# Optimization experiments

Measured on AMD Instinct MI355X. Metric: run time of the kernel, lower is better.

The kernel has to match this reference:

```python
import jax, jax.numpy as jnp
import numpy as np
from jax import lax

B_, L_, D_ = 4, 512, 512          # batch, seq_len, in_dim (d_model)
HID, H2 = 512, 256                # hidden_dim, per-direction LSTM width
NL, DST, DCV, DIN, DTR = 3, 16, 4, 1024, 32  # layers, d_state, d_conv, d_inner, dt_rank


def _silu(x):
    return x * jax.nn.sigmoid(x)


def _layernorm(x, g, b):
    m = x.mean(-1, keepdims=True)
    v = x.var(-1, keepdims=True)
    return (x - m) / jnp.sqrt(v + 1e-5) * g + b


def _mamba(x, wi, cw, cb, xpw, dw, db, Alog, Dp, wo):
    # x: (B,L,D)
    Bsz, Ls, _ = x.shape
    xz = jnp.einsum('bld,ed->ble', x, wi)          # (B,L,2*DIN)
    xin, z = jnp.split(xz, 2, axis=-1)
    # causal depthwise conv1d (kernel DCV, left-padded)
    xpad = jnp.pad(xin, ((0, 0), (DCV - 1, 0), (0, 0)))
    u = cb + sum(xpad[:, k:k + Ls, :] * cw[:, k] for k in range(DCV))
    u = _silu(u)                                   # (B,L,DIN)
    xdbl = jnp.einsum('blc,ec->ble', u, xpw)       # (B,L,DTR+2*DST)
    dt_in = xdbl[..., :DTR]
    Bc = xdbl[..., DTR:DTR + DST]
    Cc = xdbl[..., DTR + DST:]
    dt = jax.nn.softplus(jnp.einsum('blr,cr->blc', dt_in, dw) + db)  # (B,L,DIN)
    A = -jnp.exp(Alog)                             # (DIN,DST), negative

    def step(h, inp):
        dt_t, B_t, C_t, u_t = inp                  # (B,DIN),(B,DST),(B,DST),(B,DIN)
        dA = jnp.exp(dt_t[..., None] * A)          # (B,DIN,DST)
        h = dA * h + (dt_t * u_t)[..., None] * B_t[:, None, :]
        y = jnp.einsum('bcn,bn->bc', h, C_t)
        return h, y

    h0 = jnp.zeros((Bsz, DIN, DST), x.dtype)
    _, ys = lax.scan(step, h0, (dt.transpose(1, 0, 2), Bc.transpose(1, 0, 2),
                                Cc.transpose(1, 0, 2), u.transpose(1, 0, 2)))
    y = ys.transpose(1, 0, 2) + u * Dp
    y = y * _silu(z)
    return jnp.einsum('blc,dc->bld', y, wo)


def _lstm_dir(x, wih, whh, bih, bhh, reverse):
    Bsz = x.shape[0]

    def step(carry, xt):
        h, c = carry
        g = xt @ wih.T + h @ whh.T + bih + bhh     # (B,4*H2), PyTorch gate order i,f,g,o
        i, f, gg, o = jnp.split(g, 4, axis=-1)
        c = jax.nn.sigmoid(f) * c + jax.nn.sigmoid(i) * jnp.tanh(gg)
        h = jax.nn.sigmoid(o) * jnp.tanh(c)
        return (h, c), h

    init = (jnp.zeros((Bsz, H2), x.dtype), jnp.zeros((Bsz, H2), x.dtype))
    _, hs = lax.scan(step, init, x.transpose(1, 0, 2), reverse=reverse)
    return hs.transpose(1, 0, 2)


def setup_inputs():
    key = jax.random.key(0)
    ks = jax.random.split(key, 16)
    rn = lambda k, s, sc=0.02: jax.random.normal(k, s, jnp.float32) * sc
    inp = {}
    inp['x'] = jax.random.normal(ks[0], (B_, L_, D_), jnp.float32)
    inp['in_proj_w'] = rn(ks[1], (NL, 2 * DIN, D_))
    inp['conv_w'] = rn(ks[2], (NL, DIN, DCV), 0.2)
    inp['conv_b'] = jnp.zeros((NL, DIN), jnp.float32)
    inp['x_proj_w'] = rn(ks[3], (NL, DTR + 2 * DST, DIN))
    inp['dt_proj_w'] = rn(ks[4], (NL, DIN, DTR), 0.1)
    inp['dt_proj_b'] = jnp.full((NL, DIN), -4.0, jnp.float32)
    inp['A_log'] = jnp.log(jnp.broadcast_to(jnp.arange(1, DST + 1, dtype=jnp.float32), (NL, DIN, DST)))
    inp['D_param'] = jnp.ones((NL, DIN), jnp.float32)
    inp['out_proj_w'] = rn(ks[5], (NL, D_, DIN))
    inp['ln_g'] = jnp.ones((NL, D_), jnp.float32)
    inp['ln_b'] = jnp.zeros((NL, D_), jnp.float32)
    inp['lstm_w_ih'] = rn(ks[6], (2, 4 * H2, D_), 0.05)
    inp['lstm_w_hh'] = rn(ks[7], (2, 4 * H2, H2), 0.05)
    inp['lstm_b_ih'] = jnp.zeros((2, 4 * H2), jnp.float32)
    inp['lstm_b_hh'] = jnp.zeros((2, 4 * H2), jnp.float32)
    inp['fusion_w'] = rn(ks[8], (HID, D_ + HID), 0.02)
    inp['fusion_b'] = jnp.zeros((HID,), jnp.float32)
    return inp


def reference(x, in_proj_w, conv_w, conv_b, x_proj_w, dt_proj_w, dt_proj_b, A_log,
              D_param, out_proj_w, ln_g, ln_b, lstm_w_ih, lstm_w_hh, lstm_b_ih,
              lstm_b_hh, fusion_w, fusion_b):
    m = x
    for i in range(NL):
        mo = _mamba(m, in_proj_w[i], conv_w[i], conv_b[i], x_proj_w[i],
                    dt_proj_w[i], dt_proj_b[i], A_log[i], D_param[i], out_proj_w[i])
        m = _layernorm(m + mo, ln_g[i], ln_b[i])
    lf = _lstm_dir(x, lstm_w_ih[0], lstm_w_hh[0], lstm_b_ih[0], lstm_b_hh[0], False)
    lb = _lstm_dir(x, lstm_w_ih[1], lstm_w_hh[1], lstm_b_ih[1], lstm_b_hh[1], True)
    comb = jnp.concatenate([m, lf, lb], axis=-1)   # (B,L,D_+HID)
    return comb @ fusion_w.T + fusion_b
```

## Files before the change

### kernel.cpp

```cpp
#include <hip/hip_runtime.h>
#include <math.h>

#define B_  4
#define L_  512
#define D_  512
#define DIN 1024
#define DST 16
#define DCV 4
#define DTR 32
#define NL  3
#define H2  256

typedef _Float16 __f16;
typedef __f16 f16x2 __attribute__((ext_vector_type(2)));
typedef __f16 half8 __attribute__((ext_vector_type(8)));
typedef float f32x4v __attribute__((ext_vector_type(4)));
typedef unsigned uint4v __attribute__((ext_vector_type(4)));

__device__ __forceinline__ float fast_sigmoid(float x) { return 1.f / (1.f + __expf(-x)); }
__device__ __forceinline__ float fast_tanh(float x) { return 2.f / (1.f + __expf(-2.f * x)) - 1.f; }

__device__ __forceinline__ float dot2f(unsigned a, unsigned b, float c) {
  return __builtin_amdgcn_fdot2(__builtin_bit_cast(f16x2, a),
                                __builtin_bit_cast(f16x2, b), c, false);
}
__device__ __forceinline__ unsigned packf16(float a, float b) {
  f16x2 p; p.x = (__f16)a; p.y = (__f16)b;
  return __builtin_bit_cast(unsigned, p);
}

template<bool ACC>
__global__ __launch_bounds__(256) void gemm_mfma(
    const float* __restrict__ A, const float* __restrict__ W, float* __restrict__ C,
    int M, int N, int K, int lda, int ldb, int ldc,
    const float* __restrict__ bias, const float* __restrict__ bias2)
{
  __shared__ uint4v As[1024];
  __shared__ uint4v Bs[1024];
  const int tid  = threadIdx.x;
  const int lane = tid & 63, wid = tid >> 6;
  const int wr = wid >> 1, wc = wid & 1;
  const int fr = lane & 15, fq = lane >> 4;
  const int m0 = blockIdx.y * 128, n0 = blockIdx.x * 128;
  const int srow = tid >> 3, skb = tid & 7;

  f32x4v acc[4][4] = {};
  for (int k0 = 0; k0 < K; k0 += 64) {
    const float* Abase = A + (size_t)m0 * lda + k0;
    const float* Bbase = W + (size_t)n0 * ldb + k0;
    #pragma unroll
    for (int i = 0; i < 4; ++i) {
      int row = srow + i * 32;
      const float4* pa = (const float4*)(Abase + (size_t)row * lda + skb * 8);
      const float4* pb = (const float4*)(Bbase + (size_t)row * ldb + skb * 8);
      float4 a0 = pa[0], a1 = pa[1];
      float4 b0 = pb[0], b1 = pb[1];
      uint4v ap, bp;
      ap.x = packf16(a0.x, a0.y); ap.y = packf16(a0.z, a0.w);
      ap.z = packf16(a1.x, a1.y); ap.w = packf16(a1.z, a1.w);
      bp.x = packf16(b0.x, b0.y); bp.y = packf16(b0.z, b0.w);
      bp.z = packf16(b1.x, b1.y); bp.w = packf16(b1.z, b1.w);
      As[row * 8 + (skb ^ (row & 7))] = ap;
      Bs[row * 8 + (skb ^ (row & 7))] = bp;
    }
    __syncthreads();
    #pragma unroll
    for (int ks = 0; ks < 2; ++ks) {
      half8 af[4], bf[4];
      #pragma unroll
      for (int mt = 0; mt < 4; ++mt) {
        int row = wr * 64 + mt * 16 + fr;
        int kb = ks * 4 + fq;
        af[mt] = __builtin_bit_cast(half8, As[row * 8 + (kb ^ (row & 7))]);
      }
      #pragma unroll
      for (int nt = 0; nt < 4; ++nt) {
        int row = wc * 64 + nt * 16 + fr;
        int kb = ks * 4 + fq;
        bf[nt] = __builtin_bit_cast(half8, Bs[row * 8 + (kb ^ (row & 7))]);
      }
      #pragma unroll
      for (int mt = 0; mt < 4; ++mt)
        #pragma unroll
        for (int nt = 0; nt < 4; ++nt)
          acc[mt][nt] = __builtin_amdgcn_mfma_f32_16x16x32_f16(af[mt], bf[nt], acc[mt][nt], 0, 0, 0);
    }
    __syncthreads();
  }
  #pragma unroll
  for (int nt = 0; nt < 4; ++nt) {
    int n = n0 + wc * 64 + nt * 16 + fr;
    float bv = (bias ? bias[n] : 0.f) + (bias2 ? bias2[n] : 0.f);
    #pragma unroll
    for (int mt = 0; mt < 4; ++mt) {
      #pragma unroll
      for (int r = 0; r < 4; ++r) {
        int m = m0 + wr * 64 + mt * 16 + fq * 4 + r;
        float v = acc[mt][nt][r] + bv;
        if (ACC) C[(size_t)m * ldc + n] += v; else C[(size_t)m * ldc + n] = v;
      }
    }
  }
}

template<int ACT>
__global__ __launch_bounds__(256) void gemm_nt(
    const float* __restrict__ A, const float* __restrict__ Bm, float* __restrict__ C,
    int M, int N, int K, int lda, int ldb, int ldc,
    const float* __restrict__ bias)
{
  __shared__ __align__(16) float As[16][64];
  __shared__ __align__(16) float Bs[16][64];
  const int tid = threadIdx.x;
  const int tx = tid & 15, ty = tid >> 4;
  const int m0 = blockIdx.y * 64, n0 = blockIdx.x * 64;
  const int r = tid >> 2, kq = (tid & 3) * 4;
  float acc[4][4] = {};
  for (int k0 = 0; k0 < K; k0 += 16) {
    float4 av = *(const float4*)(A  + (size_t)(m0 + r) * lda + (k0 + kq));
    float4 bv = *(const float4*)(Bm + (size_t)(n0 + r) * ldb + (k0 + kq));
    As[kq+0][r] = av.x; As[kq+1][r] = av.y; As[kq+2][r] = av.z; As[kq+3][r] = av.w;
    Bs[kq+0][r] = bv.x; Bs[kq+1][r] = bv.y; Bs[kq+2][r] = bv.z; Bs[kq+3][r] = bv.w;
    __syncthreads();
    #pragma unroll
    for (int kk = 0; kk < 16; ++kk) {
      float4 a = *(const float4*)(&As[kk][ty*4]);
      float4 b = *(const float4*)(&Bs[kk][tx*4]);
      float aa[4] = {a.x, a.y, a.z, a.w};
      float bb[4] = {b.x, b.y, b.z, b.w};
      #pragma unroll
      for (int i = 0; i < 4; ++i)
        #pragma unroll
        for (int j = 0; j < 4; ++j)
          acc[i][j] = fmaf(aa[i], bb[j], acc[i][j]);
    }
    __syncthreads();
  }
  #pragma unroll
  for (int i = 0; i < 4; ++i) {
    int m = m0 + ty*4 + i;
    float* cp = C + (size_t)m * ldc + n0 + tx*4;
    #pragma unroll
    for (int j = 0; j < 4; ++j) {
      int n = n0 + tx*4 + j;
      float v = acc[i][j];
      if (bias)  v += bias[n];
      if (ACT == 1) v = (v > 20.f) ? v : log1pf(__expf(v));
      cp[j] = v;
    }
  }
}

__global__ __launch_bounds__(256) void pad_xpw(
    const float* __restrict__ src, float* __restrict__ dst)
{
  int t = blockIdx.x * 256 + threadIdx.x;
  int r = t >> 10;
  dst[t] = (r < 64) ? src[t] : 0.f;
}

__global__ __launch_bounds__(256) void pack_whh(
    const float* __restrict__ whh, uint4* __restrict__ wpk)
{
  int idx = blockIdx.x * 256 + threadIdx.x;
  int t = idx & 511;
  int q = (idx >> 9) & 15;
  int G = (idx >> 13) & 3;
  int dir = idx >> 15;
  int j = t >> 1, ks = t & 1;
  const float* src = whh + (size_t)dir * 262144 + (size_t)(G * 256 + j) * 256 + ks * 128 + q * 8;
  float4 fa = ((const float4*)src)[0];
  float4 fb = ((const float4*)src)[1];
  uint4 pk;
  pk.x = packf16(fa.x, fa.y); pk.y = packf16(fa.z, fa.w);
  pk.z = packf16(fb.x, fb.y); pk.w = packf16(fb.z, fb.w);
  wpk[idx] = pk;
}

__global__ __launch_bounds__(256) void conv_silu(
    const float* __restrict__ xz, const float* __restrict__ cw, const float* __restrict__ cb,
    float* __restrict__ u)
{
  int t = blockIdx.x * 256 + threadIdx.x;
  int c  = t & (DIN - 1);
  int bl = t >> 10;
  int l  = bl & (L_ - 1);
  float acc = cb[c];
  #pragma unroll
  for (int k = 0; k < DCV; ++k) {
    int ls = l + k - (DCV - 1);
    if (ls >= 0)
      acc = fmaf(xz[(size_t)(bl + k - (DCV - 1)) * 2048 + c], cw[c * DCV + k], acc);
  }
  u[t] = acc * fast_sigmoid(acc);
}

__global__ __launch_bounds__(256) void scan_kernel(
    const float* __restrict__ dt, const float* __restrict__ u,
    const float* __restrict__ xdbl, const float* __restrict__ xz,
    const float* __restrict__ A_log, const float* __restrict__ Dp,
    float* __restrict__ y)
{
  int t = blockIdx.x * 256 + threadIdx.x;
  int n  = t & 15;
  int bc = t >> 4;
  int c  = bc & (DIN - 1);
  int b  = bc >> 10;
  float Ac = -__expf(A_log[c * DST + n]);
  float Dc = Dp[c];
  float h = 0.f;
  const size_t row = (size_t)b * L_;

#define DECLP(i) float dtv##i, uv##i, Bn##i, Cn##i, zv##i;
  DECLP(0) DECLP(1) DECLP(2) DECLP(3)
#define LOADP(i, l) { \
    const size_t nb_ = row + (l); \
    dtv##i = dt[nb_ * DIN + c]; \
    uv##i  = u [nb_ * DIN + c]; \
    Bn##i  = xdbl[nb_ * 128 + 32 + n]; \
    Cn##i  = xdbl[nb_ * 128 + 48 + n]; \
    zv##i  = xz[nb_ * 2048 + 1024 + c]; }
#define STEPP(i, l) { \
    float dA_ = __expf(dtv##i * Ac); \
    h = fmaf(dA_, h, (dtv##i * uv##i) * Bn##i); \
    float p_ = h * Cn##i; \
    p_ += __shfl_xor(p_, 1, 64); \
    p_ += __shfl_xor(p_, 2, 64); \
    p_ += __shfl_xor(p_, 4, 64); \
    p_ += __shfl_xor(p_, 8, 64); \
    if (n == 0) { \
      float yv_ = p_ + uv##i * Dc; \
      yv_ *= zv##i * fast_sigmoid(zv##i); \
      y[(row + (l)) * DIN + c] = yv_; \
    } }

  LOADP(0, 0) LOADP(1, 1) LOADP(2, 2) LOADP(3, 3)
  for (int l = 0; l < L_ - 4; l += 4) {
    STEPP(0, l)     LOADP(0, l + 4)
    STEPP(1, l + 1) LOADP(1, l + 5)
    STEPP(2, l + 2) LOADP(2, l + 6)
    STEPP(3, l + 3) LOADP(3, l + 7)
  }
  STEPP(0, L_ - 4) STEPP(1, L_ - 3) STEPP(2, L_ - 2) STEPP(3, L_ - 1)
#undef DECLP
#undef LOADP
#undef STEPP
}

__global__ __launch_bounds__(64) void resid_ln(
    const float* __restrict__ a, const float* __restrict__ mo,
    const float* __restrict__ g, const float* __restrict__ bta,
    float* __restrict__ outm, int ldo)
{
  int row = blockIdx.x;
  int lane = threadIdx.x;
  const float* pa = a  + (size_t)row * 512;
  const float* pb = mo + (size_t)row * 512;
  float v[8];
  float s = 0.f, s2 = 0.f;
  #pragma unroll
  for (int i = 0; i < 8; ++i) {
    float x = pa[lane + i * 64] + pb[lane + i * 64];
    v[i] = x; s += x; s2 += x * x;
  }
  #pragma unroll
  for (int off = 1; off < 64; off <<= 1) {
    s  += __shfl_xor(s,  off, 64);
    s2 += __shfl_xor(s2, off, 64);
  }
  float mean = s * (1.f / 512.f);
  float var  = s2 * (1.f / 512.f) - mean * mean;
  float rstd = rsqrtf(var + 1e-5f);
  #pragma unroll
  for (int i = 0; i < 8; ++i) {
    int cidx = lane + i * 64;
    outm[(size_t)row * ldo + cidx] = (v[i] - mean) * rstd * g[cidx] + bta[cidx];
  }
}


#define WDECL(q) uint4 W0_##q, W1_##q, W2_##q;
#define LDG1(W, G, q) W = wp[((G) * 16 + (q)) * 512 + t];
#define WLOAD(q) LDG1(W0_##q, 0, q) LDG1(W1_##q, 1, q) LDG1(W2_##q, 2, q)
#define WSTEP(q) { \
    uint4 hv = h4s[buf][(q) * 2 + ks]; \
    uint4 wv = wo_lds[(q) * 512 + t]; \
    a0 = dot2f(W0_##q.x, hv.x, a0); a0 = dot2f(W0_##q.y, hv.y, a0); \
    a0 = dot2f(W0_##q.z, hv.z, a0); a0 = dot2f(W0_##q.w, hv.w, a0); \
    a1 = dot2f(W1_##q.x, hv.x, a1); a1 = dot2f(W1_##q.y, hv.y, a1); \
    a1 = dot2f(W1_##q.z, hv.z, a1); a1 = dot2f(W1_##q.w, hv.w, a1); \
    a2 = dot2f(W2_##q.x, hv.x, a2); a2 = dot2f(W2_##q.y, hv.y, a2); \
    a2 = dot2f(W2_##q.z, hv.z, a2); a2 = dot2f(W2_##q.w, hv.w, a2); \
    a3 = dot2f(wv.x, hv.x, a3); a3 = dot2f(wv.y, hv.y, a3); \
    a3 = dot2f(wv.z, hv.z, a3); a3 = dot2f(wv.w, hv.w, a3); }
#define REP16(M) M(0) M(1) M(2) M(3) M(4) M(5) M(6) M(7) \
                 M(8) M(9) M(10) M(11) M(12) M(13) M(14) M(15)

__global__ __launch_bounds__(512, 1) void lstm_rec(
    const float* __restrict__ gx, const uint4* __restrict__ wpk,
    float* __restrict__ comb)
{
  __shared__ uint4 wo_lds[16 * 512];
  __shared__ __align__(16) uint4 h4s[2][32];
  const int dir = blockIdx.x >> 2, b = blockIdx.x & 3;
  const int t = threadIdx.x;
  const int j = t >> 1, ks = t & 1;
  const uint4* wp = wpk + (size_t)dir * 4 * 16 * 512;

  REP16(WDECL)
  REP16(WLOAD)

  #pragma unroll
  for (int q = 0; q < 16; ++q)
    wo_lds[q * 512 + t] = wp[(3 * 16 + q) * 512 + t];

  if (t < 256) ((unsigned*)h4s)[t] = 0u;
  float c_reg = 0.f;
  float* outp = comb + 512 + dir * 256;
  const float* gxb = gx + (size_t)(b * L_) * 2048 + dir * 1024;
  const int offA = (ks ? 1 : 0) * 256 + j;
  const int offB = (ks ? 3 : 2) * 256 + j;
  const int p_   = t >> 2;
  const int hidx = ((p_ >> 2) & 15) * 8 + (p_ >> 6) * 4 + (p_ & 3);
  __syncthreads();

  int buf = 0;
  const int l0 = dir ? (L_ - 1) : 0;
  float pgA = gxb[(size_t)l0 * 2048 + offA];
  float pgB = gxb[(size_t)l0 * 2048 + offB];

  for (int s = 0; s < L_; ++s) {
    const int l = dir ? (L_ - 1 - s) : s;
    float pgA_n = 0.f, pgB_n = 0.f;
    if (s + 1 < L_) {
      const int ln = dir ? (L_ - 2 - s) : (s + 1);
      pgA_n = gxb[(size_t)ln * 2048 + offA];
      pgB_n = gxb[(size_t)ln * 2048 + offB];
    }
    float a0 = 0.f, a1 = 0.f, a2 = 0.f, a3 = 0.f;
    REP16(WSTEP)
    if (ks == 0) { a0 += pgA; a2 += pgB; } else { a1 += pgA; a3 += pgB; }
    a0 += __shfl_xor(a0, 1, 64);
    a1 += __shfl_xor(a1, 1, 64);
    a2 += __shfl_xor(a2, 1, 64);
    a3 += __shfl_xor(a3, 1, 64);
    const float si = fast_sigmoid(a0);
    const float sf = fast_sigmoid(a1);
    const float tg = fast_tanh(a2);
    const float so = fast_sigmoid(a3);
    c_reg = fmaf(sf, c_reg, si * tg);
    const float hv = so * fast_tanh(c_reg);
    if (ks == 0) outp[(size_t)(b * L_ + l) * 1024 + j] = hv;
    const float hv2 = __shfl_xor(hv, 2, 64);
    if ((t & 3) == 0)
      ((unsigned*)h4s[buf ^ 1])[hidx] = packf16(hv, hv2);
    pgA = pgA_n; pgB = pgB_n;
    buf ^= 1;
    __syncthreads();
  }
}

extern "C" void kernel_launch(void* const* d_in, const int* in_sizes, int n_in,
                              void* d_out, int out_size, void* d_ws, size_t ws_size,
                              hipStream_t stream)
{
  const float* x    = (const float*)d_in[0];
  const float* wi   = (const float*)d_in[1];
  const float* cw   = (const float*)d_in[2];
  const float* cb   = (const float*)d_in[3];
  const float* xpw  = (const float*)d_in[4];
  const float* dw   = (const float*)d_in[5];
  const float* db   = (const float*)d_in[6];
  const float* Alog = (const float*)d_in[7];
  const float* Dp   = (const float*)d_in[8];
  const float* wo   = (const float*)d_in[9];
  const float* lng  = (const float*)d_in[10];
  const float* lnb  = (const float*)d_in[11];
  const float* wih  = (const float*)d_in[12];
  const float* whh  = (const float*)d_in[13];
  const float* bih  = (const float*)d_in[14];
  const float* bhh  = (const float*)d_in[15];
  const float* fw   = (const float*)d_in[16];
  const float* fb   = (const float*)d_in[17];
  float* out = (float*)d_out;

  float* F    = (float*)d_ws;
  float* xz   = F;
  float* gx   = F;
  float* u    = F + 4194304;
  float* xdbl = F + 6291456;
  float* dt   = F + 6553600;
  float* ybuf = F + 8650752;
  float* mo   = F + 10747904;
  float* mbuf = F + 11796480;
  float* comb = F + 12845056;
  uint4* wpk  = (uint4*)(F + 14942208);
  float* xpw_pad = mo;

  const int M = B_ * L_;
  dim3 blk(256);

  gemm_mfma<false><<<dim3(2048/128, M/128), blk, 0, stream>>>(
      x, wih, gx, M, 2048, 512, 512, 512, 2048, bih, bhh);
  pack_whh<<<dim3(256), blk, 0, stream>>>(whh, wpk);
  lstm_rec<<<dim3(8), dim3(512), 0, stream>>>(gx, wpk, comb);

  for (int i = 0; i < NL; ++i) {
    const float* min = (i == 0) ? x : mbuf;
    pad_xpw<<<dim3(512), blk, 0, stream>>>(xpw + (size_t)i*64*1024, xpw_pad);
    gemm_mfma<false><<<dim3(2048/128, M/128), blk, 0, stream>>>(
        min, wi + (size_t)i*2048*512, xz, M, 2048, 512, 512, 512, 2048, nullptr, nullptr);
    conv_silu<<<dim3((M*DIN)/256), blk, 0, stream>>>(
        xz, cw + (size_t)i*DIN*DCV, cb + i*DIN, u);
    gemm_mfma<false><<<dim3(1, M/128), blk, 0, stream>>>(
        u, xpw_pad, xdbl, M, 128, 1024, 1024, 1024, 128, nullptr, nullptr);
    gemm_nt<1><<<dim3(1024/64, M/64), blk, 0, stream>>>(
        xdbl, dw + (size_t)i*1024*32, dt, M, 1024, 32, 128, 32, 1024, db + i*1024);
    scan_kernel<<<dim3((B_*DIN*DST)/256), blk, 0, stream>>>(
        dt, u, xdbl, xz, Alog + (size_t)i*DIN*DST, Dp + i*DIN, ybuf);
    gemm_mfma<false><<<dim3(512/128, M/128), blk, 0, stream>>>(
        ybuf, wo + (size_t)i*512*1024, mo, M, 512, 1024, 1024, 1024, 512, nullptr, nullptr);
    if (i < NL - 1)
      resid_ln<<<dim3(M), dim3(64), 0, stream>>>(
          min, mo, lng + i*512, lnb + i*512, mbuf, 512);
    else
      resid_ln<<<dim3(M), dim3(64), 0, stream>>>(
          min, mo, lng + i*512, lnb + i*512, comb, 1024);
  }

  gemm_mfma<false><<<dim3(512/128, M/128), blk, 0, stream>>>(
      comb, fw, out, M, 512, 1024, 1024, 1024, 512, fb, nullptr);
}
```

Before: 1.575 ms.

## Split LSTM recurrence across blocks with global hidden-state exchange and grid barriers

The LSTM recurrent kernel is restructured so that each of 16 blocks owns 32 hidden units for all four batch rows of one direction, rather than each of 8 blocks handling one batch row with the full weight matrix. Each block keeps its weight slice in registers, and a 16-lane shuffle reduction replaces the pairwise split. Per-step hidden states are exchanged through global memory with atomic loads and stores, and an atomic counter acts as a per-step barrier across the 8 blocks of a direction. This spreads the serial recurrence over more compute units and removes the LDS weight reads, but it adds a global synchronisation every step. It also relies on all 16 blocks being co-resident.

```diff
diff --git a/kernel.cpp b/kernel.cpp
--- a/kernel.cpp
+++ b/kernel.cpp
@@ -163,12 +163,15 @@
     const float* __restrict__ whh, uint4* __restrict__ wpk)
 {
   int idx = blockIdx.x * 256 + threadIdx.x;
-  int t = idx & 511;
-  int q = (idx >> 9) & 15;
-  int G = (idx >> 13) & 3;
-  int dir = idx >> 15;
-  int j = t >> 1, ks = t & 1;
-  const float* src = whh + (size_t)dir * 262144 + (size_t)(G * 256 + j) * 256 + ks * 128 + q * 8;
+  int u4sel = idx & 1;
+  int lane  = (idx >> 1) & 63;
+  int w     = (idx >> 7) & 7;
+  int g     = (idx >> 10) & 3;
+  int ug    = (idx >> 12) & 7;
+  int dir   = idx >> 15;
+  int j  = ug * 32 + w * 4 + (lane >> 4);
+  int ks = lane & 15;
+  const float* src = whh + (size_t)dir * 262144 + (size_t)(g * 256 + j) * 256 + ks * 16 + u4sel * 8;
   float4 fa = ((const float4*)src)[0];
   float4 fb = ((const float4*)src)[1];
   uint4 pk;
@@ -279,84 +282,112 @@
 }
 
 
-#define WDECL(q) uint4 W0_##q, W1_##q, W2_##q;
-#define LDG1(W, G, q) W = wp[((G) * 16 + (q)) * 512 + t];
-#define WLOAD(q) LDG1(W0_##q, 0, q) LDG1(W1_##q, 1, q) LDG1(W2_##q, 2, q)
-#define WSTEP(q) { \
-    uint4 hv = h4s[buf][(q) * 2 + ks]; \
-    uint4 wv = wo_lds[(q) * 512 + t]; \
-    a0 = dot2f(W0_##q.x, hv.x, a0); a0 = dot2f(W0_##q.y, hv.y, a0); \
-    a0 = dot2f(W0_##q.z, hv.z, a0); a0 = dot2f(W0_##q.w, hv.w, a0); \
-    a1 = dot2f(W1_##q.x, hv.x, a1); a1 = dot2f(W1_##q.y, hv.y, a1); \
-    a1 = dot2f(W1_##q.z, hv.z, a1); a1 = dot2f(W1_##q.w, hv.w, a1); \
-    a2 = dot2f(W2_##q.x, hv.x, a2); a2 = dot2f(W2_##q.y, hv.y, a2); \
-    a2 = dot2f(W2_##q.z, hv.z, a2); a2 = dot2f(W2_##q.w, hv.w, a2); \
-    a3 = dot2f(wv.x, hv.x, a3); a3 = dot2f(wv.y, hv.y, a3); \
-    a3 = dot2f(wv.z, hv.z, a3); a3 = dot2f(wv.w, hv.w, a3); }
-#define REP16(M) M(0) M(1) M(2) M(3) M(4) M(5) M(6) M(7) \
-                 M(8) M(9) M(10) M(11) M(12) M(13) M(14) M(15)
+#define HDECL(b) unsigned h##b##0,h##b##1,h##b##2,h##b##3,h##b##4,h##b##5,h##b##6,h##b##7;
+#define HLOAD(b) { const unsigned* hp_ = hrow + (b)*128; \
+  h##b##0 = __hip_atomic_load(hp_+0, __ATOMIC_RELAXED, __HIP_MEMORY_SCOPE_AGENT); \
+  h##b##1 = __hip_atomic_load(hp_+1, __ATOMIC_RELAXED, __HIP_MEMORY_SCOPE_AGENT); \
+  h##b##2 = __hip_atomic_load(hp_+2, __ATOMIC_RELAXED, __HIP_MEMORY_SCOPE_AGENT); \
+  h##b##3 = __hip_atomic_load(hp_+3, __ATOMIC_RELAXED, __HIP_MEMORY_SCOPE_AGENT); \
+  h##b##4 = __hip_atomic_load(hp_+4, __ATOMIC_RELAXED, __HIP_MEMORY_SCOPE_AGENT); \
+  h##b##5 = __hip_atomic_load(hp_+5, __ATOMIC_RELAXED, __HIP_MEMORY_SCOPE_AGENT); \
+  h##b##6 = __hip_atomic_load(hp_+6, __ATOMIC_RELAXED, __HIP_MEMORY_SCOPE_AGENT); \
+  h##b##7 = __hip_atomic_load(hp_+7, __ATOMIC_RELAXED, __HIP_MEMORY_SCOPE_AGENT); }
+#define DOTG(g, Wa, Wb, b) \
+  a##g##b = dot2f(Wa.x, h##b##0, a##g##b); a##g##b = dot2f(Wa.y, h##b##1, a##g##b); \
+  a##g##b = dot2f(Wa.z, h##b##2, a##g##b); a##g##b = dot2f(Wa.w, h##b##3, a##g##b); \
+  a##g##b = dot2f(Wb.x, h##b##4, a##g##b); a##g##b = dot2f(Wb.y, h##b##5, a##g##b); \
+  a##g##b = dot2f(Wb.z, h##b##6, a##g##b); a##g##b = dot2f(Wb.w, h##b##7, a##g##b);
+#define DOTB(b) DOTG(0,W0a,W0b,b) DOTG(1,W1a,W1b,b) DOTG(2,W2a,W2b,b) DOTG(3,W3a,W3b,b)
+#define RED(a) a += __shfl_xor(a,1,64); a += __shfl_xor(a,2,64); \
+               a += __shfl_xor(a,4,64); a += __shfl_xor(a,8,64);
+#define PTW(b) { \
+    float si_ = fast_sigmoid(a0##b); \
+    float sf_ = fast_sigmoid(a1##b); \
+    float tg_ = fast_tanh(a2##b); \
+    float so_ = fast_sigmoid(a3##b); \
+    c##b = fmaf(sf_, c##b, si_ * tg_); \
+    hv##b = so_ * fast_tanh(c##b); }
 
 __global__ __launch_bounds__(512, 1) void lstm_rec(
     const float* __restrict__ gx, const uint4* __restrict__ wpk,
-    float* __restrict__ comb)
-{
-  __shared__ uint4 wo_lds[16 * 512];
-  __shared__ __align__(16) uint4 h4s[2][32];
-  const int dir = blockIdx.x >> 2, b = blockIdx.x & 3;
+    float* __restrict__ comb, unsigned* __restrict__ hst, unsigned* __restrict__ cnt)
+{
+  const int bid = blockIdx.x;
+  const int dir = bid >> 3, ug = bid & 7;
   const int t = threadIdx.x;
-  const int j = t >> 1, ks = t & 1;
-  const uint4* wp = wpk + (size_t)dir * 4 * 16 * 512;
-
-  REP16(WDECL)
-  REP16(WLOAD)
-
-  #pragma unroll
-  for (int q = 0; q < 16; ++q)
-    wo_lds[q * 512 + t] = wp[(3 * 16 + q) * 512 + t];
-
-  if (t < 256) ((unsigned*)h4s)[t] = 0u;
-  float c_reg = 0.f;
-  float* outp = comb + 512 + dir * 256;
-  const float* gxb = gx + (size_t)(b * L_) * 2048 + dir * 1024;
-  const int offA = (ks ? 1 : 0) * 256 + j;
-  const int offB = (ks ? 3 : 2) * 256 + j;
-  const int p_   = t >> 2;
-  const int hidx = ((p_ >> 2) & 15) * 8 + (p_ >> 6) * 4 + (p_ & 3);
-  __syncthreads();
-
-  int buf = 0;
-  const int l0 = dir ? (L_ - 1) : 0;
-  float pgA = gxb[(size_t)l0 * 2048 + offA];
-  float pgB = gxb[(size_t)l0 * 2048 + offB];
+  const int jl = t >> 4, ks = t & 15;
+  const int j  = ug * 32 + jl;
+
+  const uint4* wsl = wpk + ((size_t)(dir * 8 + ug) * 4096);
+  const int wi_ = (t >> 6) * 128 + (t & 63) * 2;
+  uint4 W0a = wsl[0*1024 + wi_], W0b = wsl[0*1024 + wi_ + 1];
+  uint4 W1a = wsl[1*1024 + wi_], W1b = wsl[1*1024 + wi_ + 1];
+  uint4 W2a = wsl[2*1024 + wi_], W2b = wsl[2*1024 + wi_ + 1];
+  uint4 W3a = wsl[3*1024 + wi_], W3b = wsl[3*1024 + wi_ + 1];
+
+  const int g0 = ks & 3, b0 = ks >> 2;
+  float c0 = 0.f, c1 = 0.f, c2 = 0.f, c3 = 0.f;
+  const float* gxb = gx + dir * 1024 + g0 * 256 + j;
+  float* combp = comb + 512 + dir * 256 + j;
+  unsigned* hdir = hst + (size_t)dir * 512 * 512;
+  unsigned* cdir = cnt + dir * 512;
+
+  int l = dir ? (L_ - 1) : 0;
+  const int lstep = dir ? -1 : 1;
+  float gxv = gxb[(size_t)(b0 * 512 + l) * 2048];
 
   for (int s = 0; s < L_; ++s) {
-    const int l = dir ? (L_ - 1 - s) : s;
-    float pgA_n = 0.f, pgB_n = 0.f;
+    float gxn = 0.f;
+    if (s + 1 < L_) gxn = gxb[(size_t)(b0 * 512 + l + lstep) * 2048];
+
+    float a00=0,a01=0,a02=0,a03=0, a10=0,a11=0,a12=0,a13=0,
+          a20=0,a21=0,a22=0,a23=0, a30=0,a31=0,a32=0,a33=0;
+    if (s > 0) {
+      const unsigned* hrow = hdir + (size_t)(s - 1) * 512 + ks * 8;
+      HDECL(0) HDECL(1) HDECL(2) HDECL(3)
+      HLOAD(0) HLOAD(1) HLOAD(2) HLOAD(3)
+      DOTB(0) DOTB(1) DOTB(2) DOTB(3)
+    }
+    a00 += (ks== 0)?gxv:0.f; a10 += (ks== 1)?gxv:0.f; a20 += (ks== 2)?gxv:0.f; a30 += (ks== 3)?gxv:0.f;
+    a01 += (ks== 4)?gxv:0.f; a11 += (ks== 5)?gxv:0.f; a21 += (ks== 6)?gxv:0.f; a31 += (ks== 7)?gxv:0.f;
+    a02 += (ks== 8)?gxv:0.f; a12 += (ks== 9)?gxv:0.f; a22 += (ks==10)?gxv:0.f; a32 += (ks==11)?gxv:0.f;
+    a03 += (ks==12)?gxv:0.f; a13 += (ks==13)?gxv:0.f; a23 += (ks==14)?gxv:0.f; a33 += (ks==15)?gxv:0.f;
+    RED(a00) RED(a01) RED(a02) RED(a03)
+    RED(a10) RED(a11) RED(a12) RED(a13)
+    RED(a20) RED(a21) RED(a22) RED(a23)
+    RED(a30) RED(a31) RED(a32) RED(a33)
+
+    float hv0, hv1, hv2, hv3;
+    PTW(0) PTW(1) PTW(2) PTW(3)
+
+    if (ks == 0) {
+      combp[(size_t)(0 * 512 + l) * 1024] = hv0;
+      combp[(size_t)(1 * 512 + l) * 1024] = hv1;
+      combp[(size_t)(2 * 512 + l) * 1024] = hv2;
+      combp[(size_t)(3 * 512 + l) * 1024] = hv3;
+    }
+    float hp0 = __shfl_xor(hv0, 16, 64);
+    float hp1 = __shfl_xor(hv1, 16, 64);
+    float hp2 = __shfl_xor(hv2, 16, 64);
+    float hp3 = __shfl_xor(hv3, 16, 64);
+    if (ks == 0 && !(jl & 1)) {
+      unsigned* hw = hdir + (size_t)s * 512 + (j >> 1);
+      __hip_atomic_store(hw + 0*128, packf16(hv0, hp0), __ATOMIC_RELAXED, __HIP_MEMORY_SCOPE_AGENT);
+      __hip_atomic_store(hw + 1*128, packf16(hv1, hp1), __ATOMIC_RELAXED, __HIP_MEMORY_SCOPE_AGENT);
+      __hip_atomic_store(hw + 2*128, packf16(hv2, hp2), __ATOMIC_RELAXED, __HIP_MEMORY_SCOPE_AGENT);
+      __hip_atomic_store(hw + 3*128, packf16(hv3, hp3), __ATOMIC_RELAXED, __HIP_MEMORY_SCOPE_AGENT);
+    }
     if (s + 1 < L_) {
-      const int ln = dir ? (L_ - 2 - s) : (s + 1);
-      pgA_n = gxb[(size_t)ln * 2048 + offA];
-      pgB_n = gxb[(size_t)ln * 2048 + offB];
-    }
-    float a0 = 0.f, a1 = 0.f, a2 = 0.f, a3 = 0.f;
-    REP16(WSTEP)
-    if (ks == 0) { a0 += pgA; a2 += pgB; } else { a1 += pgA; a3 += pgB; }
-    a0 += __shfl_xor(a0, 1, 64);
-    a1 += __shfl_xor(a1, 1, 64);
-    a2 += __shfl_xor(a2, 1, 64);
-    a3 += __shfl_xor(a3, 1, 64);
-    const float si = fast_sigmoid(a0);
-    const float sf = fast_sigmoid(a1);
-    const float tg = fast_tanh(a2);
-    const float so = fast_sigmoid(a3);
-    c_reg = fmaf(sf, c_reg, si * tg);
-    const float hv = so * fast_tanh(c_reg);
-    if (ks == 0) outp[(size_t)(b * L_ + l) * 1024 + j] = hv;
-    const float hv2 = __shfl_xor(hv, 2, 64);
-    if ((t & 3) == 0)
-      ((unsigned*)h4s[buf ^ 1])[hidx] = packf16(hv, hv2);
-    pgA = pgA_n; pgB = pgB_n;
-    buf ^= 1;
-    __syncthreads();
+      __threadfence();
+      __syncthreads();
+      if (t == 0) {
+        atomicAdd(&cdir[s], 1u);
+        while (__hip_atomic_load(&cdir[s], __ATOMIC_ACQUIRE, __HIP_MEMORY_SCOPE_AGENT) < 8u) {}
+      }
+      __syncthreads();
+    }
+    gxv = gxn;
+    l += lstep;
   }
 }
 
@@ -395,6 +426,8 @@
   float* mbuf = F + 11796480;
   float* comb = F + 12845056;
   uint4* wpk  = (uint4*)(F + 14942208);
+  unsigned* hst = (unsigned*)dt;
+  unsigned* cnt = (unsigned*)ybuf;
   float* xpw_pad = mo;
 
   const int M = B_ * L_;
@@ -403,7 +436,8 @@
   gemm_mfma<false><<<dim3(2048/128, M/128), blk, 0, stream>>>(
       x, wih, gx, M, 2048, 512, 512, 512, 2048, bih, bhh);
   pack_whh<<<dim3(256), blk, 0, stream>>>(whh, wpk);
-  lstm_rec<<<dim3(8), dim3(512), 0, stream>>>(gx, wpk, comb);
+  hipMemsetAsync(cnt, 0, 1024 * sizeof(unsigned), stream);
+  lstm_rec<<<dim3(16), dim3(512), 0, stream>>>(gx, wpk, comb, hst, cnt);
 
   for (int i = 0; i < NL; ++i) {
     const float* min = (i == 0) ? x : mbuf;
```

Result: slower. 5.994 ms (+280.6%).

## Feed MFMA GEMMs with fp16 operands produced by upstream kernels

Applied to the files above, without the earlier changes.

Replaces the fp32-input GEMM, which converted to fp16 while staging, with a version that reads fp16 operands directly. Producers (conv_silu, scan, resid_ln, lstm_rec) now write fp16 copies of their activations, and the weights are packed to fp16 by separate kernels each call. This halves the global traffic of GEMM operand loads and removes conversion work from the GEMM inner loop. In exchange it adds extra pack launches and weight conversion traffic on every call, and rearranges the workspace layout.

```diff
diff --git a/kernel.cpp b/kernel.cpp
--- a/kernel.cpp
+++ b/kernel.cpp
@@ -30,8 +30,8 @@
 }
 
 template<bool ACC>
-__global__ __launch_bounds__(256) void gemm_mfma(
-    const float* __restrict__ A, const float* __restrict__ W, float* __restrict__ C,
+__global__ __launch_bounds__(256) void gemm_mfma_h(
+    const __f16* __restrict__ A, const __f16* __restrict__ W, float* __restrict__ C,
     int M, int N, int K, int lda, int ldb, int ldc,
     const float* __restrict__ bias, const float* __restrict__ bias2)
 {
@@ -46,20 +46,13 @@
 
   f32x4v acc[4][4] = {};
   for (int k0 = 0; k0 < K; k0 += 64) {
-    const float* Abase = A + (size_t)m0 * lda + k0;
-    const float* Bbase = W + (size_t)n0 * ldb + k0;
+    const __f16* Ab = A + (size_t)m0 * lda + k0;
+    const __f16* Bb = W + (size_t)n0 * ldb + k0;
     #pragma unroll
     for (int i = 0; i < 4; ++i) {
       int row = srow + i * 32;
-      const float4* pa = (const float4*)(Abase + (size_t)row * lda + skb * 8);
-      const float4* pb = (const float4*)(Bbase + (size_t)row * ldb + skb * 8);
-      float4 a0 = pa[0], a1 = pa[1];
-      float4 b0 = pb[0], b1 = pb[1];
-      uint4v ap, bp;
-      ap.x = packf16(a0.x, a0.y); ap.y = packf16(a0.z, a0.w);
-      ap.z = packf16(a1.x, a1.y); ap.w = packf16(a1.z, a1.w);
-      bp.x = packf16(b0.x, b0.y); bp.y = packf16(b0.z, b0.w);
-      bp.z = packf16(b1.x, b1.y); bp.w = packf16(b1.z, b1.w);
+      uint4v ap = *(const uint4v*)(Ab + (size_t)row * lda + skb * 8);
+      uint4v bp = *(const uint4v*)(Bb + (size_t)row * ldb + skb * 8);
       As[row * 8 + (skb ^ (row & 7))] = ap;
       Bs[row * 8 + (skb ^ (row & 7))] = bp;
     }
@@ -151,12 +144,21 @@
   }
 }
 
-__global__ __launch_bounds__(256) void pad_xpw(
-    const float* __restrict__ src, float* __restrict__ dst)
+__global__ __launch_bounds__(256) void packh(
+    const float* __restrict__ src, __f16* __restrict__ dst, int n)
 {
   int t = blockIdx.x * 256 + threadIdx.x;
-  int r = t >> 10;
-  dst[t] = (r < 64) ? src[t] : 0.f;
+  if (t < n) dst[t] = (__f16)src[t];
+}
+
+__global__ __launch_bounds__(256) void pack_xpw_h(
+    const float* __restrict__ xpw, __f16* __restrict__ dst)
+{
+  int t = blockIdx.x * 256 + threadIdx.x;
+  int layer = t >> 17;
+  int r = (t >> 10) & 127;
+  int k = t & 1023;
+  dst[t] = (r < 64) ? (__f16)xpw[layer * 65536 + r * 1024 + k] : (__f16)0.f;
 }
 
 __global__ __launch_bounds__(256) void pack_whh(
@@ -179,7 +181,7 @@
 
 __global__ __launch_bounds__(256) void conv_silu(
     const float* __restrict__ xz, const float* __restrict__ cw, const float* __restrict__ cb,
-    float* __restrict__ u)
+    float* __restrict__ u, __f16* __restrict__ uh)
 {
   int t = blockIdx.x * 256 + threadIdx.x;
   int c  = t & (DIN - 1);
@@ -192,14 +194,16 @@
     if (ls >= 0)
       acc = fmaf(xz[(size_t)(bl + k - (DCV - 1)) * 2048 + c], cw[c * DCV + k], acc);
   }
-  u[t] = acc * fast_sigmoid(acc);
+  float v = acc * fast_sigmoid(acc);
+  u[t] = v;
+  uh[t] = (__f16)v;
 }
 
 __global__ __launch_bounds__(256) void scan_kernel(
     const float* __restrict__ dt, const float* __restrict__ u,
     const float* __restrict__ xdbl, const float* __restrict__ xz,
     const float* __restrict__ A_log, const float* __restrict__ Dp,
-    float* __restrict__ y)
+    __f16* __restrict__ y)
 {
   int t = blockIdx.x * 256 + threadIdx.x;
   int n  = t & 15;
@@ -231,7 +235,7 @@
     if (n == 0) { \
       float yv_ = p_ + uv##i * Dc; \
       yv_ *= zv##i * fast_sigmoid(zv##i); \
-      y[(row + (l)) * DIN + c] = yv_; \
+      y[(row + (l)) * DIN + c] = (__f16)yv_; \
     } }
 
   LOADP(0, 0) LOADP(1, 1) LOADP(2, 2) LOADP(3, 3)
@@ -250,7 +254,7 @@
 __global__ __launch_bounds__(64) void resid_ln(
     const float* __restrict__ a, const float* __restrict__ mo,
     const float* __restrict__ g, const float* __restrict__ bta,
-    float* __restrict__ outm, int ldo)
+    float* __restrict__ outm, int ldo, __f16* __restrict__ outh, int ldoh)
 {
   int row = blockIdx.x;
   int lane = threadIdx.x;
@@ -274,10 +278,11 @@
   #pragma unroll
   for (int i = 0; i < 8; ++i) {
     int cidx = lane + i * 64;
-    outm[(size_t)row * ldo + cidx] = (v[i] - mean) * rstd * g[cidx] + bta[cidx];
-  }
-}
-
+    float o = (v[i] - mean) * rstd * g[cidx] + bta[cidx];
+    if (outm) outm[(size_t)row * ldo + cidx] = o;
+    outh[(size_t)row * ldoh + cidx] = (__f16)o;
+  }
+}
 
 #define WDECL(q) uint4 W0_##q, W1_##q, W2_##q;
 #define LDG1(W, G, q) W = wp[((G) * 16 + (q)) * 512 + t];
@@ -298,7 +303,7 @@
 
 __global__ __launch_bounds__(512, 1) void lstm_rec(
     const float* __restrict__ gx, const uint4* __restrict__ wpk,
-    float* __restrict__ comb)
+    __f16* __restrict__ comb)
 {
   __shared__ uint4 wo_lds[16 * 512];
   __shared__ __align__(16) uint4 h4s[2][32];
@@ -316,7 +321,7 @@
 
   if (t < 256) ((unsigned*)h4s)[t] = 0u;
   float c_reg = 0.f;
-  float* outp = comb + 512 + dir * 256;
+  __f16* outp = comb + 512 + dir * 256;
   const float* gxb = gx + (size_t)(b * L_) * 2048 + dir * 1024;
   const int offA = (ks ? 1 : 0) * 256 + j;
   const int offB = (ks ? 3 : 2) * 256 + j;
@@ -350,7 +355,7 @@
     const float so = fast_sigmoid(a3);
     c_reg = fmaf(sf, c_reg, si * tg);
     const float hv = so * fast_tanh(c_reg);
-    if (ks == 0) outp[(size_t)(b * L_ + l) * 1024 + j] = hv;
+    if (ks == 0) outp[(size_t)(b * L_ + l) * 1024 + j] = (__f16)hv;
     const float hv2 = __shfl_xor(hv, 2, 64);
     if ((t & 3) == 0)
       ((unsigned*)h4s[buf ^ 1])[hidx] = packf16(hv, hv2);
@@ -384,50 +389,64 @@
   const float* fb   = (const float*)d_in[17];
   float* out = (float*)d_out;
 
-  float* F    = (float*)d_ws;
-  float* xz   = F;
-  float* gx   = F;
-  float* u    = F + 4194304;
-  float* xdbl = F + 6291456;
-  float* dt   = F + 6553600;
-  float* ybuf = F + 8650752;
-  float* mo   = F + 10747904;
-  float* mbuf = F + 11796480;
-  float* comb = F + 12845056;
-  uint4* wpk  = (uint4*)(F + 14942208);
-  float* xpw_pad = mo;
+  float* F = (float*)d_ws;
+  float* xz     = F;
+  float* gx     = F;
+  float* mo     = F + 3145728;
+  float* u      = F + 4194304;
+  float* xdbl   = F + 7340032;
+  float* dt     = F + 7602176;
+  float* mbuf   = F + 10747904;
+  __f16* fw_h   = (__f16*)(F + 4194304);
+  __f16* u_h    = (__f16*)(F + 6291456);
+  __f16* wih_h  = (__f16*)(F + 7602176);
+  uint4* wpk    = (uint4*)(F + 8126464);
+  __f16* wi_hc  = (__f16*)(F + 8388608);
+  __f16* ybuf_h = (__f16*)(F + 9699328);
+  __f16* x_h    = (__f16*)(F + 9699328);
+  __f16* mbuf_h = (__f16*)(F + 11796480);
+  __f16* comb_h = (__f16*)(F + 12320768);
+  __f16* wo_h   = (__f16*)(F + 13369344);
+  __f16* xpw_h  = (__f16*)(F + 14155776);
 
   const int M = B_ * L_;
   dim3 blk(256);
 
-  gemm_mfma<false><<<dim3(2048/128, M/128), blk, 0, stream>>>(
-      x, wih, gx, M, 2048, 512, 512, 512, 2048, bih, bhh);
+  packh<<<dim3(4096), blk, 0, stream>>>(x,   x_h,   1048576);
+  packh<<<dim3(4096), blk, 0, stream>>>(wih, wih_h, 1048576);
+  packh<<<dim3(6144), blk, 0, stream>>>(wo,  wo_h,  1572864);
+  pack_xpw_h<<<dim3(1536), blk, 0, stream>>>(xpw, xpw_h);
+
+  gemm_mfma_h<false><<<dim3(16, 16), blk, 0, stream>>>(
+      x_h, wih_h, gx, M, 2048, 512, 512, 512, 2048, bih, bhh);
   pack_whh<<<dim3(256), blk, 0, stream>>>(whh, wpk);
-  lstm_rec<<<dim3(8), dim3(512), 0, stream>>>(gx, wpk, comb);
+  lstm_rec<<<dim3(8), dim3(512), 0, stream>>>(gx, wpk, comb_h);
 
   for (int i = 0; i < NL; ++i) {
     const float* min = (i == 0) ? x : mbuf;
-    pad_xpw<<<dim3(512), blk, 0, stream>>>(xpw + (size_t)i*64*1024, xpw_pad);
-    gemm_mfma<false><<<dim3(2048/128, M/128), blk, 0, stream>>>(
-        min, wi + (size_t)i*2048*512, xz, M, 2048, 512, 512, 512, 2048, nullptr, nullptr);
-    conv_silu<<<dim3((M*DIN)/256), blk, 0, stream>>>(
-        xz, cw + (size_t)i*DIN*DCV, cb + i*DIN, u);
-    gemm_mfma<false><<<dim3(1, M/128), blk, 0, stream>>>(
-        u, xpw_pad, xdbl, M, 128, 1024, 1024, 1024, 128, nullptr, nullptr);
-    gemm_nt<1><<<dim3(1024/64, M/64), blk, 0, stream>>>(
-        xdbl, dw + (size_t)i*1024*32, dt, M, 1024, 32, 128, 32, 1024, db + i*1024);
-    scan_kernel<<<dim3((B_*DIN*DST)/256), blk, 0, stream>>>(
-        dt, u, xdbl, xz, Alog + (size_t)i*DIN*DST, Dp + i*DIN, ybuf);
-    gemm_mfma<false><<<dim3(512/128, M/128), blk, 0, stream>>>(
-        ybuf, wo + (size_t)i*512*1024, mo, M, 512, 1024, 1024, 1024, 512, nullptr, nullptr);
+    const __f16* min_h = (i == 0) ? x_h : mbuf_h;
+    packh<<<dim3(4096), blk, 0, stream>>>(wi + (size_t)i*1048576, wi_hc, 1048576);
+    gemm_mfma_h<false><<<dim3(16, 16), blk, 0, stream>>>(
+        min_h, wi_hc, xz, M, 2048, 512, 512, 512, 2048, nullptr, nullptr);
+    conv_silu<<<dim3(8192), blk, 0, stream>>>(
+        xz, cw + (size_t)i*DIN*DCV, cb + i*DIN, u, u_h);
+    gemm_mfma_h<false><<<dim3(1, 16), blk, 0, stream>>>(
+        u_h, xpw_h + (size_t)i*131072, xdbl, M, 128, 1024, 1024, 1024, 128, nullptr, nullptr);
+    gemm_nt<1><<<dim3(16, 32), blk, 0, stream>>>(
+        xdbl, dw + (size_t)i*32768, dt, M, 1024, 32, 128, 32, 1024, db + i*1024);
+    scan_kernel<<<dim3(256), blk, 0, stream>>>(
+        dt, u, xdbl, xz, Alog + (size_t)i*DIN*DST, Dp + i*DIN, ybuf_h);
+    gemm_mfma_h<false><<<dim3(4, 16), blk, 0, stream>>>(
+        ybuf_h, wo_h + (size_t)i*524288, mo, M, 512, 1024, 1024, 1024, 512, nullptr, nullptr);
     if (i < NL - 1)
       resid_ln<<<dim3(M), dim3(64), 0, stream>>>(
-          min, mo, lng + i*512, lnb + i*512, mbuf, 512);
+          min, mo, lng + i*512, lnb + i*512, mbuf, 512, mbuf_h, 512);
     else
       resid_ln<<<dim3(M), dim3(64), 0, stream>>>(
-          min, mo, lng + i*512, lnb + i*512, comb, 1024);
-  }
-
-  gemm_mfma<false><<<dim3(512/128, M/128), blk, 0, stream>>>(
-      comb, fw, out, M, 512, 1024, 1024, 1024, 512, fb, nullptr);
-}
+          min, mo, lng + i*512, lnb + i*512, nullptr, 0, comb_h, 1024);
+  }
+
+  packh<<<dim3(2048), blk, 0, stream>>>(fw, fw_h, 524288);
+  gemm_mfma_h<false><<<dim3(4, 16), blk, 0, stream>>>(
+      comb_h, fw_h, out, M, 512, 1024, 1024, 1024, 512, fb, nullptr);
+}
```

After: 1.554 ms. No clear change (-1.3%).
